# Kernel optimization log

Measured on AMD Instinct MI355X. Metric: run time of the kernel, lower is better.

Reference implementation:

```python
import jax, jax.numpy as jnp
import numpy as np
import math

D = 2048
H = 8
DK = D // H // 2  # 128
NL = 3
EPS = 1e-6
SCALE = 1.0 / math.sqrt(DK)


def _ln(x, g, b):
    m = jnp.mean(x, axis=-1, keepdims=True)
    v = jnp.mean(jnp.square(x - m), axis=-1, keepdims=True)
    return (x - m) * jax.lax.rsqrt(v + EPS) * g + b


def _attn_layer(x, g, b, Wq, Wk, Wv):
    bs = x.shape[0]
    xn = _ln(x, g, b)
    # torch Linear: y = x @ W.T ; reshape to (bs, h, 2, d_k)
    q = (xn @ Wq.T).reshape(bs, H, 2, DK)
    k = (xn @ Wk.T).reshape(bs, H, 2, DK)
    v = (xn @ Wv.T).reshape(bs, H, 2, DK)
    s = jnp.einsum('bhpd,bhqd->bhpq', q, k) * SCALE  # tiny 2x2 scores
    a = jax.nn.softmax(s, axis=-1)
    o = jnp.einsum('bhpq,bhqd->bhpd', a, v).reshape(bs, D)
    return o + x


def _ff_layer(x, lnd_g, lnd_b, lnt_g, lnt_b, Wd1, bd1, Wd2, bd2, Wt1, bt1, Wt2, bt2):
    d, t = x[:, :D // 2], x[:, D // 2:]
    dn = _ln(d, lnd_g, lnd_b)
    tn = _ln(t, lnt_g, lnt_b)
    do = jax.nn.relu(dn @ Wd1.T + bd1) @ Wd2.T + bd2
    to = jax.nn.relu(tn @ Wt1.T + bt1) @ Wt2.T + bt2
    return jnp.concatenate([do, to], axis=-1) + x


def setup_inputs() -> dict:
    key = jax.random.key(0)
    ks = iter(jax.random.split(key, 64))
    s = 0.02
    inp = {}
    inp['x'] = jax.random.normal(next(ks), (8192, D), dtype=jnp.float32)
    # attention stacks: NL layers
    inp['attn_ln_g'] = jnp.ones((NL, D), jnp.float32)
    inp['attn_ln_b'] = jnp.zeros((NL, D), jnp.float32)
    inp['Wq'] = jax.random.normal(next(ks), (NL, D, D), jnp.float32) * s
    inp['Wk'] = jax.random.normal(next(ks), (NL, D, D), jnp.float32) * s
    inp['Wv'] = jax.random.normal(next(ks), (NL, D, D), jnp.float32) * s
    # feedforward stacks: NL-1 layers
    F = NL - 1
    hd = D // 2
    inp['ff_lnd_g'] = jnp.ones((F, hd), jnp.float32)
    inp['ff_lnd_b'] = jnp.zeros((F, hd), jnp.float32)
    inp['ff_lnt_g'] = jnp.ones((F, hd), jnp.float32)
    inp['ff_lnt_b'] = jnp.zeros((F, hd), jnp.float32)
    inp['Wd1'] = jax.random.normal(next(ks), (F, D, hd), jnp.float32) * s
    inp['bd1'] = jnp.zeros((F, D), jnp.float32)
    inp['Wd2'] = jax.random.normal(next(ks), (F, hd, D), jnp.float32) * s
    inp['bd2'] = jnp.zeros((F, hd), jnp.float32)
    inp['Wt1'] = jax.random.normal(next(ks), (F, D, hd), jnp.float32) * s
    inp['bt1'] = jnp.zeros((F, D), jnp.float32)
    inp['Wt2'] = jax.random.normal(next(ks), (F, hd, D), jnp.float32) * s
    inp['bt2'] = jnp.zeros((F, hd), jnp.float32)
    # output head
    inp['Wo1'] = jax.random.normal(next(ks), (hd, D), jnp.float32) * s
    inp['bo1'] = jnp.zeros((hd,), jnp.float32)
    inp['Wo2'] = jax.random.normal(next(ks), (1, hd), jnp.float32) * s
    inp['bo2'] = jnp.zeros((1,), jnp.float32)
    return inp


def reference(x, attn_ln_g, attn_ln_b, Wq, Wk, Wv,
              ff_lnd_g, ff_lnd_b, ff_lnt_g, ff_lnt_b,
              Wd1, bd1, Wd2, bd2, Wt1, bt1, Wt2, bt2,
              Wo1, bo1, Wo2, bo2):
    for n in range(NL - 1):
        x = _attn_layer(x, attn_ln_g[n], attn_ln_b[n], Wq[n], Wk[n], Wv[n])
        x = _ff_layer(x, ff_lnd_g[n], ff_lnd_b[n], ff_lnt_g[n], ff_lnt_b[n],
                      Wd1[n], bd1[n], Wd2[n], bd2[n], Wt1[n], bt1[n], Wt2[n], bt2[n])
    x = _attn_layer(x, attn_ln_g[-1], attn_ln_b[-1], Wq[-1], Wk[-1], Wv[-1])
    h = jax.nn.relu(x @ Wo1.T + bo1)
    return h @ Wo2.T + bo2  # [bs, 1]
```

## Files before the change

kernel.cpp:

```cpp
#include <hip/hip_runtime.h>
#include <stdint.h>


typedef __bf16 bf16x8 __attribute__((ext_vector_type(8)));
typedef float f32x4 __attribute__((ext_vector_type(4)));

static __device__ __forceinline__ float bf2f(unsigned short u) {
  unsigned int x = ((unsigned int)u) << 16;
  float f;
  __builtin_memcpy(&f, &x, 4);
  return f;
}
static __device__ __forceinline__ unsigned short f2bf(float f) {
  unsigned int x;
  __builtin_memcpy(&x, &f, 4);
  x += 0x7fffu + ((x >> 16) & 1u);
  return (unsigned short)(x >> 16);
}

static __device__ __forceinline__ void gload_lds16(const void* g, void* l) {
  __builtin_amdgcn_global_load_lds(
      (const __attribute__((address_space(1))) unsigned int*)g,
      (__attribute__((address_space(3))) unsigned int*)l, 16, 0, 0);
}

__global__ __launch_bounds__(256) void cvt_kernel(
    const float* __restrict__ in, unsigned short* __restrict__ out, long n) {
  const long i = ((long)blockIdx.x * 256 + threadIdx.x) * 4;
  if (i + 3 < n) {
    float4 f = *(const float4*)(in + i);
    *(ushort4*)(out + i) = make_ushort4(f2bf(f.x), f2bf(f.y), f2bf(f.z), f2bf(f.w));
  }
}

__global__ __launch_bounds__(512, 2) void gemm8_kernel(
    const unsigned short* __restrict__ A, int lda,
    const unsigned short* __restrict__ B, int K,
    void* __restrict__ Cp, int ldc, const float* __restrict__ bias,
    int relu, int out_f32, int resadd,
    const unsigned short* __restrict__ A2, const unsigned short* __restrict__ B2,
    void* __restrict__ C2p, const float* __restrict__ bias2, int dual) {
  extern __shared__ __align__(16) char smem[];

  const int tid = threadIdx.x;
  const int lane = tid & 63;
  const int w = tid >> 6;
  const int wm = w >> 2;
  const int wn = w & 3;
  const long brow = (long)blockIdx.y * 256;

  const unsigned short* Ap = A;
  const unsigned short* Bp = B;
  const float* bi = bias;
  void* Cq = Cp;
  long bcol;
  if (dual && (int)blockIdx.x >= (int)(gridDim.x >> 1)) {
    Ap = A2; Bp = B2; bi = bias2; Cq = C2p;
    bcol = (long)(blockIdx.x - (gridDim.x >> 1)) * 256;
  } else {
    bcol = (long)blockIdx.x * 256;
  }

  const int NT = K >> 6;

  auto stageA = [&](int t, int h) {
    char* lb = smem + (t & 1) * 65536 + h * 16384 + (tid & ~63) * 16;
    const unsigned short* g0 = Ap + (brow + h * 128) * (long)lda + (long)t * 64;
#pragma unroll
    for (int j = 0; j < 2; ++j) {
      const int u = j * 512 + tid;
      const int lrow = u >> 3;
      const int scb = ((u & 7) * 16) ^ ((lrow & 7) << 4);
      gload_lds16((const char*)(g0 + (long)lrow * lda) + scb, lb + j * 8192);
    }
  };
  auto stageB = [&](int t, int h) {
    char* lb = smem + (t & 1) * 65536 + 32768 + h * 16384 + (tid & ~63) * 16;
    const unsigned short* g0 = Bp + (bcol + h * 128) * (long)K + (long)t * 64;
#pragma unroll
    for (int j = 0; j < 2; ++j) {
      const int u = j * 512 + tid;
      const int lrow = u >> 3;
      const int scb = ((u & 7) * 16) ^ ((lrow & 7) << 4);
      gload_lds16((const char*)(g0 + (long)lrow * K) + scb, lb + j * 8192);
    }
  };

  f32x4 acc[8][4];
  const f32x4 fz = {0.f, 0.f, 0.f, 0.f};
#pragma unroll
  for (int m = 0; m < 8; ++m)
#pragma unroll
    for (int n = 0; n < 4; ++n) acc[m][n] = fz;

  const int frow = lane & 15;
  const int fkb = (lane >> 4) * 16;
  const int fswz = (lane & 7) << 4;

  stageA(0, 0); stageA(0, 1); stageB(0, 0); stageB(0, 1);
  if (NT > 1) { stageA(1, 0); stageA(1, 1); stageB(1, 0); stageB(1, 1); }
  asm volatile("s_waitcnt vmcnt(8)");
  __builtin_amdgcn_s_barrier();

  for (int t = 0; t < NT; ++t) {
    char* Ab = smem + (t & 1) * 65536;
    char* Bb = Ab + 32768;

    bf16x8 af[8][2], bfv[4][2];
#pragma unroll
    for (int m = 0; m < 8; ++m)
#pragma unroll
      for (int kk = 0; kk < 2; ++kk)
        af[m][kk] = *(const bf16x8*)(Ab + (wm * 128 + m * 16 + frow) * 128 +
                                     ((kk * 64 + fkb) ^ fswz));
#pragma unroll
    for (int n = 0; n < 4; ++n)
#pragma unroll
      for (int kk = 0; kk < 2; ++kk)
        bfv[n][kk] = *(const bf16x8*)(Bb + (wn * 64 + n * 16 + frow) * 128 +
                                      ((kk * 64 + fkb) ^ fswz));
    __builtin_amdgcn_s_barrier();
    asm volatile("s_waitcnt lgkmcnt(0)");
    __builtin_amdgcn_sched_barrier(0);
    __builtin_amdgcn_s_setprio(1);
#pragma unroll
    for (int m = 0; m < 4; ++m)
#pragma unroll
      for (int n = 0; n < 2; ++n)
#pragma unroll
        for (int kk = 0; kk < 2; ++kk)
          acc[m][n] = __builtin_amdgcn_mfma_f32_16x16x32_bf16(
              af[m][kk], bfv[n][kk], acc[m][n], 0, 0, 0);
    __builtin_amdgcn_s_setprio(0);
    __builtin_amdgcn_s_barrier();

    if (t + 2 < NT) stageA(t + 2, 0);
    __builtin_amdgcn_s_barrier();
    __builtin_amdgcn_s_setprio(1);
#pragma unroll
    for (int m = 0; m < 4; ++m)
#pragma unroll
      for (int n = 2; n < 4; ++n)
#pragma unroll
        for (int kk = 0; kk < 2; ++kk)
          acc[m][n] = __builtin_amdgcn_mfma_f32_16x16x32_bf16(
              af[m][kk], bfv[n][kk], acc[m][n], 0, 0, 0);
    __builtin_amdgcn_s_setprio(0);
    __builtin_amdgcn_s_barrier();

    if (t + 2 < NT) stageB(t + 2, 0);
    __builtin_amdgcn_s_barrier();
    __builtin_amdgcn_s_setprio(1);
#pragma unroll
    for (int m = 4; m < 8; ++m)
#pragma unroll
      for (int n = 0; n < 2; ++n)
#pragma unroll
        for (int kk = 0; kk < 2; ++kk)
          acc[m][n] = __builtin_amdgcn_mfma_f32_16x16x32_bf16(
              af[m][kk], bfv[n][kk], acc[m][n], 0, 0, 0);
    __builtin_amdgcn_s_setprio(0);
    __builtin_amdgcn_s_barrier();

    if (t + 2 < NT) {
      stageA(t + 2, 1); stageB(t + 2, 1);
      asm volatile("s_waitcnt vmcnt(8)");
    } else {
      asm volatile("s_waitcnt vmcnt(0)");
    }
    __builtin_amdgcn_s_barrier();
    __builtin_amdgcn_s_setprio(1);
#pragma unroll
    for (int m = 4; m < 8; ++m)
#pragma unroll
      for (int n = 2; n < 4; ++n)
#pragma unroll
        for (int kk = 0; kk < 2; ++kk)
          acc[m][n] = __builtin_amdgcn_mfma_f32_16x16x32_bf16(
              af[m][kk], bfv[n][kk], acc[m][n], 0, 0, 0);
    __builtin_amdgcn_s_setprio(0);
    __builtin_amdgcn_s_barrier();
  }

  const long rb0 = brow + wm * 128 + (lane >> 4) * 4;
  const long cb0 = bcol + wn * 64 + (lane & 15);
#pragma unroll
  for (int m = 0; m < 8; ++m) {
#pragma unroll
    for (int n = 0; n < 4; ++n) {
      const long col = cb0 + n * 16;
      const float bv = bi ? bi[col] : 0.f;
#pragma unroll
      for (int j = 0; j < 4; ++j) {
        const long r = rb0 + m * 16 + j;
        float v = acc[m][n][j] + bv;
        if (relu) v = fmaxf(v, 0.f);
        if (out_f32) {
          float* cp = (float*)Cq + r * (long)ldc + col;
          if (resadd) v += *cp;
          *cp = v;
        } else {
          ((unsigned short*)Cq)[r * (long)ldc + col] = f2bf(v);
        }
      }
    }
  }
}

__global__ __launch_bounds__(256) void gemm_bt_kernel(
    const unsigned short* __restrict__ A, int lda,
    const unsigned short* __restrict__ B, int K,
    void* __restrict__ Cp, int ldc,
    const float* __restrict__ bias,
    const void* __restrict__ res, int res_mode, int ldres,
    int relu, int out_f32) {
  __shared__ __align__(16) unsigned short As[128 * 32];
  __shared__ __align__(16) unsigned short Bs[128 * 32];

  const int t = threadIdx.x;
  const int lane = t & 63;
  const int w = t >> 6;
  const int wr = (w >> 1) * 64;
  const int wc = (w & 1) * 64;
  const long brow = (long)blockIdx.y * 128;
  const long bcol = (long)blockIdx.x * 128;

  const int srow = lane >> 2;
  const int scol = (lane & 3) * 8;
  const unsigned short* Ab = A + (brow + w * 32 + srow) * (long)lda + scol;
  const unsigned short* Bb = B + (bcol + w * 32 + srow) * (long)K + scol;
  unsigned short* Asb = &As[(w * 32) * 32];
  unsigned short* Bsb = &Bs[(w * 32) * 32];

  f32x4 acc[4][4];
  const f32x4 fzero = {0.f, 0.f, 0.f, 0.f};
#pragma unroll
  for (int m = 0; m < 4; ++m)
#pragma unroll
    for (int n = 0; n < 4; ++n) acc[m][n] = fzero;

  const int fr = lane & 15;
  const int fk = (lane >> 4) * 8;

  for (int kt = 0; kt < K; kt += 32) {
    gload_lds16(Ab + kt, Asb);
    gload_lds16(Ab + 16 * (long)lda + kt, Asb + 16 * 32);
    gload_lds16(Bb + kt, Bsb);
    gload_lds16(Bb + 16 * (long)K + kt, Bsb + 16 * 32);
    __syncthreads();

    bf16x8 af[4], bfv[4];
#pragma unroll
    for (int m = 0; m < 4; ++m)
      af[m] = *(const bf16x8*)&As[(wr + m * 16 + fr) * 32 + fk];
#pragma unroll
    for (int n = 0; n < 4; ++n)
      bfv[n] = *(const bf16x8*)&Bs[(wc + n * 16 + fr) * 32 + fk];
#pragma unroll
    for (int m = 0; m < 4; ++m)
#pragma unroll
      for (int n = 0; n < 4; ++n)
        acc[m][n] = __builtin_amdgcn_mfma_f32_16x16x32_bf16(af[m], bfv[n],
                                                            acc[m][n], 0, 0, 0);
    __syncthreads();
  }

  const long rbase = brow + wr + (lane >> 4) * 4;
#pragma unroll
  for (int m = 0; m < 4; ++m) {
#pragma unroll
    for (int n = 0; n < 4; ++n) {
      const long col = bcol + wc + n * 16 + fr;
      const float bv = bias ? bias[col] : 0.f;
#pragma unroll
      for (int j = 0; j < 4; ++j) {
        const long r = rbase + m * 16 + j;
        float v = acc[m][n][j] + bv;
        if (relu) v = fmaxf(v, 0.f);
        if (res_mode == 1)
          v += ((const float*)res)[r * (long)ldres + col];
        else if (res_mode == 2)
          v += bf2f(((const unsigned short*)res)[r * (long)ldres + col]);
        if (out_f32)
          ((float*)Cp)[r * (long)ldc + col] = v;
        else
          ((unsigned short*)Cp)[r * (long)ldc + col] = f2bf(v);
      }
    }
  }
}

template <int L>
__global__ __launch_bounds__(256) void ln_kernel(
    const void* __restrict__ inp, int in_bf16, int ldin,
    const float* __restrict__ g, const float* __restrict__ b,
    unsigned short* __restrict__ outp, int ldout) {
  constexpr int VEC = L / 256;
  const long row = blockIdx.x;
  const int t = threadIdx.x;
  float v[VEC];
  if (in_bf16) {
    const unsigned short* p = (const unsigned short*)inp + row * (long)ldin + t * VEC;
#pragma unroll
    for (int i = 0; i < VEC; i += 4) {
      ushort4 u = *(const ushort4*)(p + i);
      v[i] = bf2f(u.x); v[i + 1] = bf2f(u.y); v[i + 2] = bf2f(u.z); v[i + 3] = bf2f(u.w);
    }
  } else {
    const float* p = (const float*)inp + row * (long)ldin + t * VEC;
#pragma unroll
    for (int i = 0; i < VEC; i += 4) {
      float4 f = *(const float4*)(p + i);
      v[i] = f.x; v[i + 1] = f.y; v[i + 2] = f.z; v[i + 3] = f.w;
    }
  }
  float s = 0.f, sq = 0.f;
#pragma unroll
  for (int i = 0; i < VEC; ++i) { s += v[i]; sq += v[i] * v[i]; }
#pragma unroll
  for (int off = 32; off; off >>= 1) {
    s += __shfl_xor(s, off, 64);
    sq += __shfl_xor(sq, off, 64);
  }
  __shared__ float red[8];
  if ((t & 63) == 0) { red[t >> 6] = s; red[4 + (t >> 6)] = sq; }
  __syncthreads();
  s = red[0] + red[1] + red[2] + red[3];
  sq = red[4] + red[5] + red[6] + red[7];
  const float mean = s * (1.f / L);
  const float var = sq * (1.f / L) - mean * mean;
  const float rstd = rsqrtf(var + 1e-6f);
  unsigned short* op = outp + row * (long)ldout + t * VEC;
  const float* gp = g + t * VEC;
  const float* bp = b + t * VEC;
#pragma unroll
  for (int i = 0; i < VEC; i += 4) {
    float4 gg = *(const float4*)(gp + i);
    float4 bb = *(const float4*)(bp + i);
    *(ushort4*)(op + i) = make_ushort4(
        f2bf((v[i + 0] - mean) * rstd * gg.x + bb.x),
        f2bf((v[i + 1] - mean) * rstd * gg.y + bb.y),
        f2bf((v[i + 2] - mean) * rstd * gg.z + bb.z),
        f2bf((v[i + 3] - mean) * rstd * gg.w + bb.w));
  }
}

__global__ __launch_bounds__(512) void attn_glue_kernel(
    const unsigned short* __restrict__ Q, const unsigned short* __restrict__ Kq,
    const unsigned short* __restrict__ V, int ld, const void* __restrict__ Xres,
    int res_bf16, void* __restrict__ Xout, int out_bf16,
    unsigned short* __restrict__ Xout_bf) {
  const long row = blockIdx.x;
  const int h = threadIdx.x >> 6;
  const int lane = threadIdx.x & 63;
  const long qbase = row * (long)ld + h * 256;
  const long xbase = row * 2048 + h * 256;
  const int d = lane * 2;

  ushort2 q0 = *(const ushort2*)&Q[qbase + d];
  ushort2 q1 = *(const ushort2*)&Q[qbase + 128 + d];
  ushort2 k0 = *(const ushort2*)&Kq[qbase + d];
  ushort2 k1 = *(const ushort2*)&Kq[qbase + 128 + d];
  ushort2 v0 = *(const ushort2*)&V[qbase + d];
  ushort2 v1 = *(const ushort2*)&V[qbase + 128 + d];

  const float q0x = bf2f(q0.x), q0y = bf2f(q0.y);
  const float q1x = bf2f(q1.x), q1y = bf2f(q1.y);
  const float k0x = bf2f(k0.x), k0y = bf2f(k0.y);
  const float k1x = bf2f(k1.x), k1y = bf2f(k1.y);

  float s00 = q0x * k0x + q0y * k0y;
  float s01 = q0x * k1x + q0y * k1y;
  float s10 = q1x * k0x + q1y * k0y;
  float s11 = q1x * k1x + q1y * k1y;
#pragma unroll
  for (int off = 32; off; off >>= 1) {
    s00 += __shfl_xor(s00, off, 64);
    s01 += __shfl_xor(s01, off, 64);
    s10 += __shfl_xor(s10, off, 64);
    s11 += __shfl_xor(s11, off, 64);
  }
  const float SC = 0.088388347648318447f;
  s00 *= SC; s01 *= SC; s10 *= SC; s11 *= SC;
  const float m0 = fmaxf(s00, s01), m1 = fmaxf(s10, s11);
  const float e00 = __expf(s00 - m0), e01 = __expf(s01 - m0);
  const float e10 = __expf(s10 - m1), e11 = __expf(s11 - m1);
  const float i0 = 1.f / (e00 + e01), i1 = 1.f / (e10 + e11);
  const float a00 = e00 * i0, a01 = e01 * i0;
  const float a10 = e10 * i1, a11 = e11 * i1;

  const float v0x = bf2f(v0.x), v0y = bf2f(v0.y);
  const float v1x = bf2f(v1.x), v1y = bf2f(v1.y);
  float o0x = a00 * v0x + a01 * v1x, o0y = a00 * v0y + a01 * v1y;
  float o1x = a10 * v0x + a11 * v1x, o1y = a10 * v0y + a11 * v1y;

  if (res_bf16) {
    const unsigned short* xr = (const unsigned short*)Xres + xbase;
    ushort2 ra = *(const ushort2*)&xr[d];
    ushort2 rb = *(const ushort2*)&xr[128 + d];
    o0x += bf2f(ra.x); o0y += bf2f(ra.y); o1x += bf2f(rb.x); o1y += bf2f(rb.y);
  } else {
    const float* xr = (const float*)Xres + xbase;
    float2 ra = *(const float2*)&xr[d];
    float2 rb = *(const float2*)&xr[128 + d];
    o0x += ra.x; o0y += ra.y; o1x += rb.x; o1y += rb.y;
  }
  if (out_bf16) {
    unsigned short* xo = (unsigned short*)Xout + xbase;
    *(ushort2*)&xo[d] = make_ushort2(f2bf(o0x), f2bf(o0y));
    *(ushort2*)&xo[128 + d] = make_ushort2(f2bf(o1x), f2bf(o1y));
  } else {
    float* xo = (float*)Xout + xbase;
    *(float2*)&xo[d] = make_float2(o0x, o0y);
    *(float2*)&xo[128 + d] = make_float2(o1x, o1y);
  }
  if (Xout_bf) {
    unsigned short* xb = Xout_bf + xbase;
    *(ushort2*)&xb[d] = make_ushort2(f2bf(o0x), f2bf(o0y));
    *(ushort2*)&xb[128 + d] = make_ushort2(f2bf(o1x), f2bf(o1y));
  }
}

__global__ __launch_bounds__(256) void final_matvec_kernel(
    const unsigned short* __restrict__ Hm, const float* __restrict__ wv,
    const float* __restrict__ b2, float* __restrict__ outp) {
  const long row = blockIdx.x;
  const int t = threadIdx.x;
  ushort4 hv = *(const ushort4*)&Hm[row * 1024 + t * 4];
  float4 wq = *(const float4*)&wv[t * 4];
  float s = bf2f(hv.x) * wq.x + bf2f(hv.y) * wq.y +
            bf2f(hv.z) * wq.z + bf2f(hv.w) * wq.w;
#pragma unroll
  for (int off = 32; off; off >>= 1) s += __shfl_xor(s, off, 64);
  __shared__ float red[4];
  if ((t & 63) == 0) red[t >> 6] = s;
  __syncthreads();
  if (t == 0) outp[row] = red[0] + red[1] + red[2] + red[3] + b2[0];
}

extern "C" void kernel_launch(void* const* d_in, const int* in_sizes, int n_in,
                              void* d_out, int out_size, void* d_ws,
                              size_t ws_size, hipStream_t stream) {
  const float* x_in = (const float*)d_in[0];
  const float* aln_g = (const float*)d_in[1];
  const float* aln_b = (const float*)d_in[2];
  const float* Wq_f = (const float*)d_in[3];
  const float* Wk_f = (const float*)d_in[4];
  const float* Wv_f = (const float*)d_in[5];
  const float* lnd_g = (const float*)d_in[6];
  const float* lnd_b = (const float*)d_in[7];
  const float* lnt_g = (const float*)d_in[8];
  const float* lnt_b = (const float*)d_in[9];
  const float* Wd1_f = (const float*)d_in[10];
  const float* bd1 = (const float*)d_in[11];
  const float* Wd2_f = (const float*)d_in[12];
  const float* bd2 = (const float*)d_in[13];
  const float* Wt1_f = (const float*)d_in[14];
  const float* bt1 = (const float*)d_in[15];
  const float* Wt2_f = (const float*)d_in[16];
  const float* bt2 = (const float*)d_in[17];
  const float* Wo1_f = (const float*)d_in[18];
  const float* bo1 = (const float*)d_in[19];
  const float* Wo2_f = (const float*)d_in[20];
  const float* bo2 = (const float*)d_in[21];

  const size_t R = 8192, D = 2048, HD = 1024;
  const size_t DD = D * D;
  const size_t WALL = (3 * 3 * DD + 4 * 2 * D * HD + HD * D) * 2;
  const size_t SLOT = 3 * DD * 2;
  const size_t ACT = R * D * 4 + R * D * 2 + R * 6144 * 2;

  auto cvt = [&](const float* src, unsigned short* dst, long n) {
    cvt_kernel<<<dim3((unsigned)(n / 1024)), dim3(256), 0, stream>>>(src, dst, n);
  };

  if (ws_size >= ACT + SLOT) {
    const bool planAll = ws_size >= ACT + WALL;
    hipFuncSetAttribute(reinterpret_cast<const void*>(gemm8_kernel),
                        hipFuncAttributeMaxDynamicSharedMemorySize, 131072);

    char* p = (char*)d_ws;
    float* Xf = (float*)p; p += R * D * 4;
    unsigned short* XN = (unsigned short*)p; p += R * D * 2;
    unsigned short* QKVb = (unsigned short*)p; p += R * 6144 * 2;
    unsigned short* Warea = (unsigned short*)p;

    unsigned short* H1d = QKVb;
    unsigned short* H1t = QKVb + R * 2048;
    unsigned short* Hfin = QKVb + R * 4096;
    unsigned short* DN = XN;
    unsigned short* TN = XN + R * HD;

    unsigned short* Wqkv_b = Warea;
    unsigned short* Wd1_b = Wqkv_b + 9 * DD;
    unsigned short* Wt1_b = Wd1_b + 2 * D * HD;
    unsigned short* Wd2_b = Wt1_b + 2 * D * HD;
    unsigned short* Wt2_b = Wd2_b + 2 * D * HD;
    unsigned short* Wo1_b = Wt2_b + 2 * D * HD;
    if (planAll) {
      for (int n = 0; n < 3; ++n) {
        cvt(Wq_f + n * DD, Wqkv_b + n * 3 * DD + 0 * DD, DD);
        cvt(Wk_f + n * DD, Wqkv_b + n * 3 * DD + 1 * DD, DD);
        cvt(Wv_f + n * DD, Wqkv_b + n * 3 * DD + 2 * DD, DD);
      }
      cvt(Wd1_f, Wd1_b, 2 * D * HD);
      cvt(Wt1_f, Wt1_b, 2 * D * HD);
      cvt(Wd2_f, Wd2_b, 2 * D * HD);
      cvt(Wt2_f, Wt2_b, 2 * D * HD);
      cvt(Wo1_f, Wo1_b, HD * D);
    }

    auto gemm8 = [&](const unsigned short* A, int lda, const unsigned short* B,
                     int N, int K, void* C, int ldc, const float* bias,
                     int relu, int of32, int resadd, const unsigned short* A2,
                     const unsigned short* B2, void* C2, const float* bias2) {
      dim3 grid(N / 256, 32);
      gemm8_kernel<<<grid, dim3(512), 131072, stream>>>(
          A, lda, B, K, C, ldc, bias, relu, of32, resadd, A2, B2, C2, bias2,
          A2 != nullptr);
    };

    for (int n = 0; n < 3; ++n) {
      ln_kernel<2048><<<8192, 256, 0, stream>>>(
          (n == 0) ? (const void*)x_in : (const void*)Xf, 0, 2048,
          aln_g + n * D, aln_b + n * D, XN, 2048);
      const unsigned short* Wqkv;
      if (planAll) {
        Wqkv = Wqkv_b + (size_t)n * 3 * DD;
      } else {
        cvt(Wq_f + n * DD, Warea + 0 * DD, DD);
        cvt(Wk_f + n * DD, Warea + 1 * DD, DD);
        cvt(Wv_f + n * DD, Warea + 2 * DD, DD);
        Wqkv = Warea;
      }
      gemm8(XN, 2048, Wqkv, 6144, 2048, QKVb, 6144, nullptr, 0, 0, 0,
            nullptr, nullptr, nullptr, nullptr);
      attn_glue_kernel<<<8192, 512, 0, stream>>>(
          QKVb, QKVb + 2048, QKVb + 4096, 6144,
          (n == 0) ? (const void*)x_in : (const void*)Xf, 0, Xf, 0,
          (n == 2) ? XN : nullptr);

      if (n < 2) {
        const size_t fo = (size_t)n * D * HD;
        ln_kernel<1024><<<8192, 256, 0, stream>>>(Xf, 0, 2048, lnd_g + n * HD,
                                                  lnd_b + n * HD, DN, 1024);
        ln_kernel<1024><<<8192, 256, 0, stream>>>(Xf + HD, 0, 2048,
                                                  lnt_g + n * HD,
                                                  lnt_b + n * HD, TN, 1024);
        const unsigned short *w1d, *w1t, *w2d, *w2t;
        if (planAll) {
          w1d = Wd1_b + fo; w1t = Wt1_b + fo; w2d = Wd2_b + fo; w2t = Wt2_b + fo;
        } else {
          cvt(Wd1_f + fo, Warea + 0 * D * HD, D * HD);
          cvt(Wt1_f + fo, Warea + 1 * D * HD, D * HD);
          cvt(Wd2_f + fo, Warea + 2 * D * HD, D * HD);
          cvt(Wt2_f + fo, Warea + 3 * D * HD, D * HD);
          w1d = Warea; w1t = Warea + D * HD; w2d = Warea + 2 * D * HD;
          w2t = Warea + 3 * D * HD;
        }
        gemm8(DN, 1024, w1d, 2048, 1024, H1d, 2048, bd1 + n * D, 1, 0, 0,
              nullptr, nullptr, nullptr, nullptr);
        gemm8(TN, 1024, w1t, 2048, 1024, H1t, 2048, bt1 + n * D, 1, 0, 0,
              nullptr, nullptr, nullptr, nullptr);
        gemm8(H1d, 2048, w2d, 2048, 2048, Xf, 2048, bd2 + n * HD, 0, 1, 1,
              H1t, w2t, Xf + HD, bt2 + n * HD);
      }
    }

    const unsigned short* Wo1p;
    if (planAll) {
      Wo1p = Wo1_b;
    } else {
      cvt(Wo1_f, Warea, HD * D);
      Wo1p = Warea;
    }
    gemm_bt_kernel<<<dim3(1024 / 128, 8192 / 128), dim3(256), 0, stream>>>(
        XN, 2048, Wo1p, 2048, Hfin, 1024, bo1, nullptr, 0, 0, 1, 0);
    final_matvec_kernel<<<8192, 256, 0, stream>>>(Hfin, Wo2_f, bo2,
                                                  (float*)d_out);
    return;
  }

  const size_t PLB = R * D * 2;
  const size_t XFZ = R * D * 4;
  const size_t SLOT1 = DD * 2;
  const bool planAll = ws_size >= XFZ + 4 * PLB + WALL;
  const bool xIsF32 = planAll || ws_size >= XFZ + 4 * PLB + SLOT1;

  char* p = (char*)d_ws;
  float* Xf = nullptr;
  unsigned short* Xb = nullptr;
  if (xIsF32) { Xf = (float*)p; p += XFZ; } else { Xb = (unsigned short*)p; p += PLB; }
  unsigned short* XN = (unsigned short*)p; p += PLB;
  unsigned short* Qb = (unsigned short*)p; p += PLB;
  unsigned short* Kb = (unsigned short*)p; p += PLB;
  unsigned short* Vb = (unsigned short*)p; p += PLB;
  unsigned short* Warea = (unsigned short*)p;

  void* X = xIsF32 ? (void*)Xf : (void*)Xb;
  const int xres_mode = xIsF32 ? 1 : 2;
  unsigned short* H1 = Qb;
  unsigned short* DN = XN;
  unsigned short* TN = XN + R * HD;
  unsigned short* Hfin = Vb;

  unsigned short* Wq_b = Warea;
  unsigned short* Wk_b = Wq_b + 3 * DD;
  unsigned short* Wv_b = Wk_b + 3 * DD;
  unsigned short* Wd1_b = Wv_b + 3 * DD;
  unsigned short* Wd2_b = Wd1_b + 2 * D * HD;
  unsigned short* Wt1_b = Wd2_b + 2 * D * HD;
  unsigned short* Wt2_b = Wt1_b + 2 * D * HD;
  unsigned short* Wo1_b = Wt2_b + 2 * D * HD;
  if (planAll) {
    cvt(Wq_f, Wq_b, 3 * DD);
    cvt(Wk_f, Wk_b, 3 * DD);
    cvt(Wv_f, Wv_b, 3 * DD);
    cvt(Wd1_f, Wd1_b, 2 * D * HD);
    cvt(Wd2_f, Wd2_b, 2 * D * HD);
    cvt(Wt1_f, Wt1_b, 2 * D * HD);
    cvt(Wt2_f, Wt2_b, 2 * D * HD);
    cvt(Wo1_f, Wo1_b, HD * D);
  }
  auto wbf = [&](const float* src_base, unsigned short* pre_base, size_t off,
                 size_t cnt) -> const unsigned short* {
    if (planAll) return pre_base + off;
    cvt(src_base + off, Warea, (long)cnt);
    return Warea;
  };
  auto gemm = [&](const unsigned short* A, int lda, const unsigned short* B,
                  int N, int K, void* C, int ldc, const float* bias,
                  const void* res, int res_mode, int ldres, int relu, int of32) {
    dim3 grid(N / 128, 8192 / 128);
    gemm_bt_kernel<<<grid, dim3(256), 0, stream>>>(
        A, lda, B, K, C, ldc, bias, res, res_mode, ldres, relu, of32);
  };

  for (int n = 0; n < 3; ++n) {
    const void* lin = (n == 0) ? (const void*)x_in : (const void*)X;
    const int lin_bf16 = (n == 0) ? 0 : (xIsF32 ? 0 : 1);
    ln_kernel<2048><<<8192, 256, 0, stream>>>(lin, lin_bf16, 2048,
                                              aln_g + n * D, aln_b + n * D, XN, 2048);
    const size_t wo = (size_t)n * DD;
    gemm(XN, 2048, wbf(Wq_f, Wq_b, wo, DD), 2048, 2048, Qb, 2048,
         nullptr, nullptr, 0, 0, 0, 0);
    gemm(XN, 2048, wbf(Wk_f, Wk_b, wo, DD), 2048, 2048, Kb, 2048,
         nullptr, nullptr, 0, 0, 0, 0);
    gemm(XN, 2048, wbf(Wv_f, Wv_b, wo, DD), 2048, 2048, Vb, 2048,
         nullptr, nullptr, 0, 0, 0, 0);
    attn_glue_kernel<<<8192, 512, 0, stream>>>(
        Qb, Kb, Vb, 2048, (n == 0) ? (const void*)x_in : (const void*)X,
        (n == 0) ? 0 : (xIsF32 ? 0 : 1), X, xIsF32 ? 0 : 1,
        (n == 2 && xIsF32) ? XN : nullptr);

    if (n < 2) {
      const size_t fo = (size_t)n * D * HD;
      ln_kernel<1024><<<8192, 256, 0, stream>>>(X, !xIsF32, 2048,
                                                lnd_g + n * HD, lnd_b + n * HD, DN, 1024);
      const void* Xt = xIsF32 ? (const void*)(Xf + HD) : (const void*)(Xb + HD);
      ln_kernel<1024><<<8192, 256, 0, stream>>>(Xt, !xIsF32, 2048,
                                                lnt_g + n * HD, lnt_b + n * HD, TN, 1024);
      void* Xd2 = X;
      void* Xt2 = xIsF32 ? (void*)(Xf + HD) : (void*)(Xb + HD);
      gemm(DN, 1024, wbf(Wd1_f, Wd1_b, fo, D * HD), 2048, 1024, H1, 2048,
           bd1 + n * D, nullptr, 0, 0, 1, 0);
      gemm(H1, 2048, wbf(Wd2_f, Wd2_b, fo, D * HD), 1024, 2048, Xd2, 2048,
           bd2 + n * HD, Xd2, xres_mode, 2048, 0, xIsF32 ? 1 : 0);
      gemm(TN, 1024, wbf(Wt1_f, Wt1_b, fo, D * HD), 2048, 1024, H1, 2048,
           bt1 + n * D, nullptr, 0, 0, 1, 0);
      gemm(H1, 2048, wbf(Wt2_f, Wt2_b, fo, D * HD), 1024, 2048, Xt2, 2048,
           bt2 + n * HD, Xt2, xres_mode, 2048, 0, xIsF32 ? 1 : 0);
    }
  }

  const unsigned short* Afin = xIsF32 ? XN : Xb;
  gemm(Afin, 2048, wbf(Wo1_f, Wo1_b, 0, HD * D), 1024, 2048, Hfin, 1024,
       bo1, nullptr, 0, 0, 1, 0);
  final_matvec_kernel<<<8192, 256, 0, stream>>>(Hfin, Wo2_f, bo2, (float*)d_out);
}
```

Baseline: 1.330 ms.

## Split LDS fragment loads across MFMA phases, merge FF up-projections, use gemm8 for head

The GEMM main loop now loads the A and B fragments in halves, interleaved with the four MFMA phases, instead of loading every fragment up front. The global-to-LDS staging for the next tile is regrouped: all of B goes after the second phase and all of A after the third. This is meant to lower register pressure and overlap LDS reads with matrix work. The two FF first-layer GEMMs are merged into one dual launch, the dual second-layer call's grid and N now cover both halves, and the output-head GEMM moves from the older gemm_bt kernel to gemm8. This adds more barriers and waits per iteration and relies on the dual-mode indexing being correct.

```diff
diff --git a/kernel.cpp b/kernel.cpp
--- a/kernel.cpp
+++ b/kernel.cpp
@@ -105,20 +105,20 @@
   for (int t = 0; t < NT; ++t) {
     char* Ab = smem + (t & 1) * 65536;
     char* Bb = Ab + 32768;
-
-    bf16x8 af[8][2], bfv[4][2];
-#pragma unroll
-    for (int m = 0; m < 8; ++m)
+    bf16x8 afL[4][2], afH[4][2], bfvL[2][2], bfvH[2][2];
+
+#pragma unroll
+    for (int m = 0; m < 4; ++m)
 #pragma unroll
       for (int kk = 0; kk < 2; ++kk)
-        af[m][kk] = *(const bf16x8*)(Ab + (wm * 128 + m * 16 + frow) * 128 +
-                                     ((kk * 64 + fkb) ^ fswz));
-#pragma unroll
-    for (int n = 0; n < 4; ++n)
+        afL[m][kk] = *(const bf16x8*)(Ab + (wm * 128 + m * 16 + frow) * 128 +
+                                      ((kk * 64 + fkb) ^ fswz));
+#pragma unroll
+    for (int n = 0; n < 2; ++n)
 #pragma unroll
       for (int kk = 0; kk < 2; ++kk)
-        bfv[n][kk] = *(const bf16x8*)(Bb + (wn * 64 + n * 16 + frow) * 128 +
-                                      ((kk * 64 + fkb) ^ fswz));
+        bfvL[n][kk] = *(const bf16x8*)(Bb + (wn * 64 + n * 16 + frow) * 128 +
+                                       ((kk * 64 + fkb) ^ fswz));
     __builtin_amdgcn_s_barrier();
     asm volatile("s_waitcnt lgkmcnt(0)");
     __builtin_amdgcn_sched_barrier(0);
@@ -130,40 +130,55 @@
 #pragma unroll
         for (int kk = 0; kk < 2; ++kk)
           acc[m][n] = __builtin_amdgcn_mfma_f32_16x16x32_bf16(
-              af[m][kk], bfv[n][kk], acc[m][n], 0, 0, 0);
+              afL[m][kk], bfvL[n][kk], acc[m][n], 0, 0, 0);
     __builtin_amdgcn_s_setprio(0);
     __builtin_amdgcn_s_barrier();
 
-    if (t + 2 < NT) stageA(t + 2, 0);
-    __builtin_amdgcn_s_barrier();
+#pragma unroll
+    for (int n = 0; n < 2; ++n)
+#pragma unroll
+      for (int kk = 0; kk < 2; ++kk)
+        bfvH[n][kk] = *(const bf16x8*)(Bb + (wn * 64 + (n + 2) * 16 + frow) * 128 +
+                                       ((kk * 64 + fkb) ^ fswz));
+    __builtin_amdgcn_s_barrier();
+    asm volatile("s_waitcnt lgkmcnt(0)");
+    __builtin_amdgcn_sched_barrier(0);
     __builtin_amdgcn_s_setprio(1);
 #pragma unroll
     for (int m = 0; m < 4; ++m)
 #pragma unroll
-      for (int n = 2; n < 4; ++n)
+      for (int n = 0; n < 2; ++n)
 #pragma unroll
         for (int kk = 0; kk < 2; ++kk)
-          acc[m][n] = __builtin_amdgcn_mfma_f32_16x16x32_bf16(
-              af[m][kk], bfv[n][kk], acc[m][n], 0, 0, 0);
+          acc[m][n + 2] = __builtin_amdgcn_mfma_f32_16x16x32_bf16(
+              afL[m][kk], bfvH[n][kk], acc[m][n + 2], 0, 0, 0);
     __builtin_amdgcn_s_setprio(0);
     __builtin_amdgcn_s_barrier();
 
-    if (t + 2 < NT) stageB(t + 2, 0);
-    __builtin_amdgcn_s_barrier();
+#pragma unroll
+    for (int m = 0; m < 4; ++m)
+#pragma unroll
+      for (int kk = 0; kk < 2; ++kk)
+        afH[m][kk] = *(const bf16x8*)(Ab + (wm * 128 + (m + 4) * 16 + frow) * 128 +
+                                      ((kk * 64 + fkb) ^ fswz));
+    if (t + 2 < NT) { stageB(t + 2, 0); stageB(t + 2, 1); }
+    __builtin_amdgcn_s_barrier();
+    asm volatile("s_waitcnt lgkmcnt(0)");
+    __builtin_amdgcn_sched_barrier(0);
     __builtin_amdgcn_s_setprio(1);
 #pragma unroll
-    for (int m = 4; m < 8; ++m)
+    for (int m = 0; m < 4; ++m)
 #pragma unroll
       for (int n = 0; n < 2; ++n)
 #pragma unroll
         for (int kk = 0; kk < 2; ++kk)
-          acc[m][n] = __builtin_amdgcn_mfma_f32_16x16x32_bf16(
-              af[m][kk], bfv[n][kk], acc[m][n], 0, 0, 0);
+          acc[m + 4][n] = __builtin_amdgcn_mfma_f32_16x16x32_bf16(
+              afH[m][kk], bfvL[n][kk], acc[m + 4][n], 0, 0, 0);
     __builtin_amdgcn_s_setprio(0);
     __builtin_amdgcn_s_barrier();
 
     if (t + 2 < NT) {
-      stageA(t + 2, 1); stageB(t + 2, 1);
+      stageA(t + 2, 0); stageA(t + 2, 1);
       asm volatile("s_waitcnt vmcnt(8)");
     } else {
       asm volatile("s_waitcnt vmcnt(0)");
@@ -171,13 +186,13 @@
     __builtin_amdgcn_s_barrier();
     __builtin_amdgcn_s_setprio(1);
 #pragma unroll
-    for (int m = 4; m < 8; ++m)
-#pragma unroll
-      for (int n = 2; n < 4; ++n)
+    for (int m = 0; m < 4; ++m)
+#pragma unroll
+      for (int n = 0; n < 2; ++n)
 #pragma unroll
         for (int kk = 0; kk < 2; ++kk)
-          acc[m][n] = __builtin_amdgcn_mfma_f32_16x16x32_bf16(
-              af[m][kk], bfv[n][kk], acc[m][n], 0, 0, 0);
+          acc[m + 4][n + 2] = __builtin_amdgcn_mfma_f32_16x16x32_bf16(
+              afH[m][kk], bfvH[n][kk], acc[m + 4][n + 2], 0, 0, 0);
     __builtin_amdgcn_s_setprio(0);
     __builtin_amdgcn_s_barrier();
   }
@@ -514,10 +529,11 @@
                      int N, int K, void* C, int ldc, const float* bias,
                      int relu, int of32, int resadd, const unsigned short* A2,
                      const unsigned short* B2, void* C2, const float* bias2) {
-      dim3 grid(N / 256, 32);
+      const int dual = (A2 != nullptr);
+      dim3 grid((dual ? 2 : 1) * (N / 256), 32);
       gemm8_kernel<<<grid, dim3(512), 131072, stream>>>(
           A, lda, B, K, C, ldc, bias, relu, of32, resadd, A2, B2, C2, bias2,
-          A2 != nullptr);
+          dual);
     };
 
     for (int n = 0; n < 3; ++n) {
@@ -559,10 +575,8 @@
           w2t = Warea + 3 * D * HD;
         }
         gemm8(DN, 1024, w1d, 2048, 1024, H1d, 2048, bd1 + n * D, 1, 0, 0,
-              nullptr, nullptr, nullptr, nullptr);
-        gemm8(TN, 1024, w1t, 2048, 1024, H1t, 2048, bt1 + n * D, 1, 0, 0,
-              nullptr, nullptr, nullptr, nullptr);
-        gemm8(H1d, 2048, w2d, 2048, 2048, Xf, 2048, bd2 + n * HD, 0, 1, 1,
+              TN, w1t, H1t, bt1 + n * D);
+        gemm8(H1d, 2048, w2d, 1024, 2048, Xf, 2048, bd2 + n * HD, 0, 1, 1,
               H1t, w2t, Xf + HD, bt2 + n * HD);
       }
     }
@@ -574,8 +588,8 @@
       cvt(Wo1_f, Warea, HD * D);
       Wo1p = Warea;
     }
-    gemm_bt_kernel<<<dim3(1024 / 128, 8192 / 128), dim3(256), 0, stream>>>(
-        XN, 2048, Wo1p, 2048, Hfin, 1024, bo1, nullptr, 0, 0, 1, 0);
+    gemm8(XN, 2048, Wo1p, 1024, 2048, Hfin, 1024, bo1, 1, 0, 0,
+          nullptr, nullptr, nullptr, nullptr);
     final_matvec_kernel<<<8192, 256, 0, stream>>>(Hfin, Wo2_f, bo2,
                                                   (float*)d_out);
     return;
```

Result: no change. 1.313 ms (-1.3%).
